# Performance work log

Measured on AMD Instinct MI355X. Metric: run time of the kernel, lower is better.

Reference implementation:

```python
import jax, jax.numpy as jnp
import numpy as np

N = 100000   # nodes
E = 1600000  # edges (avg degree 16)
D = 128      # input feature dim
H = 128      # Config.hidden_dim
G = 64       # graphs in batch
OUT = 2      # output classes


def setup_inputs() -> dict:
    key = jax.random.key(0)
    ks = jax.random.split(key, 12)
    s = 0.05
    return {
        "x": jax.random.normal(ks[0], (N, D), dtype=jnp.float32),
        "edge_index": jax.random.randint(ks[1], (2, E), 0, N),
        "batch": jnp.sort(jax.random.randint(ks[2], (N,), 0, G)),
        "W1": jax.random.normal(ks[3], (H, D), dtype=jnp.float32) * s,
        "b1": jnp.zeros((H,), jnp.float32),
        "W2": jax.random.normal(ks[4], (H, H), dtype=jnp.float32) * s,
        "b2": jnp.zeros((H,), jnp.float32),
        "Wf1": jax.random.normal(ks[5], (H, H), dtype=jnp.float32) * s,
        "bf1": jnp.zeros((H,), jnp.float32),
        "Wf2": jax.random.normal(ks[6], (OUT, H), dtype=jnp.float32) * s,
        "bf2": jnp.zeros((OUT,), jnp.float32),
    }


def _gnn_layer(x, src, dst, W, b):
    # message(x_j) = Linear(x[src]); linear commutes with gather, so transform
    # node features once (N rows) instead of per-edge (E rows): same math.
    xw = x @ W.T + b                                   # [N, H]
    msg = xw[src]                                      # [E, H] gather
    summed = jax.ops.segment_sum(msg, dst, num_segments=N)            # [N, H]
    cnt = jax.ops.segment_sum(jnp.ones((src.shape[0],), x.dtype), dst,
                              num_segments=N)                          # [N]
    return summed / jnp.maximum(cnt, 1.0)[:, None]     # scatter-mean (0 for deg-0)


def reference(x, edge_index, batch, W1, b1, W2, b2, Wf1, bf1, Wf2, bf2):
    src, dst = edge_index[0], edge_index[1]
    h = jax.nn.relu(_gnn_layer(x, src, dst, W1, b1))
    h = jax.nn.relu(_gnn_layer(h, src, dst, W2, b2))
    g = jax.ops.segment_max(h, batch, num_segments=G)  # global_max_pool [G, H]
    z = jax.nn.relu(g @ Wf1.T + bf1)                   # fc (dropout = identity, eval)
    z = z @ Wf2.T + bf2                                # [G, OUT]
    return jax.nn.log_softmax(z, axis=1)
```

## Files before the change

### kernel.cpp

```cpp
#include <hip/hip_runtime.h>
#include <hip/hip_fp16.h>
#include <math.h>


#define SPLIT 16
#define BUCKET_SHIFT 8
#define BUCKET_SIZE 256
#define MAXBUCK 512
#define BIN_CHUNK 4096
#define CAP 4608
#define LSTR 136

typedef _Float16 half8 __attribute__((ext_vector_type(8)));
typedef _Float16 half4v __attribute__((ext_vector_type(4)));
typedef _Float16 half2v __attribute__((ext_vector_type(2)));
typedef float floatx4 __attribute__((ext_vector_type(4)));
typedef float floatx2 __attribute__((ext_vector_type(2)));

#define RFL(v) __builtin_amdgcn_readfirstlane(v)

__global__ void k_init(int* bcur, int* gstart, int* gend, int G, int nbuck) {
    int i = threadIdx.x;
    if (i < nbuck) bcur[i] = i * CAP;
    if (i < G) { gstart[i] = 0; gend[i] = 0; }
}

__global__ __launch_bounds__(256) void k_bin(
        const int* __restrict__ src, const int* __restrict__ dst,
        int* __restrict__ bcur, int* __restrict__ staging,
        const int* __restrict__ batch, int* __restrict__ gstart,
        int* __restrict__ gend, int E, int N, int nbuck) {
    __shared__ int lh[MAXBUCK];
    __shared__ int lbase[MAXBUCK];
    __shared__ int lc[MAXBUCK];
    int t = threadIdx.x;
    for (int i = t; i < nbuck; i += 256) { lh[i] = 0; lc[i] = 0; }

    int n = blockIdx.x * 256 + t;
    if (n < N) {
        int b = batch[n];
        if (n == 0 || batch[n - 1] != b) gstart[b] = n;
        if (n == N - 1 || batch[n + 1] != b) gend[b] = n + 1;
    }
    __syncthreads();

    int base = blockIdx.x * BIN_CHUNK;
    if (base + BIN_CHUNK <= E) {
        int ds[16], ss[16];
        const int4* dv = (const int4*)(dst + base);
        const int4* sv = (const int4*)(src + base);
        #pragma unroll
        for (int j = 0; j < 4; ++j) {
            int4 d = dv[j * 256 + t];
            int4 s = sv[j * 256 + t];
            ds[j * 4 + 0] = d.x; ds[j * 4 + 1] = d.y;
            ds[j * 4 + 2] = d.z; ds[j * 4 + 3] = d.w;
            ss[j * 4 + 0] = s.x; ss[j * 4 + 1] = s.y;
            ss[j * 4 + 2] = s.z; ss[j * 4 + 3] = s.w;
        }
        #pragma unroll
        for (int q = 0; q < 16; ++q)
            atomicAdd(&lh[ds[q] >> BUCKET_SHIFT], 1);
        __syncthreads();
        for (int i = t; i < nbuck; i += 256)
            if (lh[i]) lbase[i] = atomicAdd(&bcur[i], lh[i]);
        __syncthreads();
        #pragma unroll
        for (int q = 0; q < 16; ++q) {
            int d = ds[q];
            int b = d >> BUCKET_SHIFT;
            int pos = lbase[b] + atomicAdd(&lc[b], 1);
            if (pos < (b + 1) * CAP)
                staging[pos] = ss[q] | ((d & (BUCKET_SIZE - 1)) << 24);
        }
    } else {
        int end = E;
        for (int e = base + t; e < end; e += 256)
            atomicAdd(&lh[dst[e] >> BUCKET_SHIFT], 1);
        __syncthreads();
        for (int i = t; i < nbuck; i += 256)
            if (lh[i]) lbase[i] = atomicAdd(&bcur[i], lh[i]);
        __syncthreads();
        for (int e = base + t; e < end; e += 256) {
            int d = dst[e];
            int b = d >> BUCKET_SHIFT;
            int pos = lbase[b] + atomicAdd(&lc[b], 1);
            if (pos < (b + 1) * CAP)
                staging[pos] = src[e] | ((d & (BUCKET_SIZE - 1)) << 24);
        }
    }
}

__global__ __launch_bounds__(BUCKET_SIZE) void k_bcsr(
        const int* __restrict__ staging, const int* __restrict__ bcur,
        int* __restrict__ esrc, int* __restrict__ rowstart,
        int* __restrict__ deg, int N) {
    __shared__ int lh[BUCKET_SIZE];
    __shared__ int lcur[BUCKET_SIZE];
    __shared__ int ws[4];
    int b = blockIdx.x;
    int s = b * CAP;
    int e = min(bcur[b], s + CAP);
    int t = threadIdx.x;
    lh[t] = 0;
    __syncthreads();
    for (int i = s + t; i < e; i += BUCKET_SIZE)
        atomicAdd(&lh[((unsigned)staging[i]) >> 24], 1);
    __syncthreads();
    int v = lh[t];
    int lane = t & 63;
    int wv = t >> 6;
    int inc = v;
    #pragma unroll
    for (int off = 1; off < 64; off <<= 1) {
        int x = __shfl_up(inc, off, 64);
        if (lane >= off) inc += x;
    }
    if (lane == 63) ws[wv] = inc;
    __syncthreads();
    int woff = 0;
    #pragma unroll
    for (int k = 0; k < 3; ++k)
        if (k < wv) woff += ws[k];
    int excl = woff + inc - v;
    int node = b * BUCKET_SIZE + t;
    if (node < N) { rowstart[node] = s + excl; deg[node] = v; }
    lcur[t] = excl;
    __syncthreads();
    for (int i = s + t; i < e; i += BUCKET_SIZE) {
        int p = staging[i];
        int local = ((unsigned)p) >> 24;
        int pos = atomicAdd(&lcur[local], 1);
        esrc[s + pos] = p & 0xFFFFFF;
    }
}

template <typename T>
__global__ __launch_bounds__(512) void k_gemm(const T* __restrict__ in,
                                              const float* __restrict__ W,
                                              const float* __restrict__ bias,
                                              unsigned char* __restrict__ out8,
                                              int N) {
    __shared__ _Float16 sX[128 * LSTR];
    __shared__ _Float16 sW[128 * LSTR];
    int t = threadIdx.x;
    int n0 = blockIdx.x * 128;

    #pragma unroll
    for (int it = 0; it < 8; ++it) {
        int lin = it * 512 + t;
        int r = lin >> 5;
        int c = (lin & 31) * 4;
        half4v xh;
        int n = n0 + r;
        if (n < N) {
            if constexpr (sizeof(T) == 4) {
                float4 xv = *(const float4*)((const float*)in + (size_t)n * 128 + c);
                xh = half4v{ (_Float16)xv.x, (_Float16)xv.y, (_Float16)xv.z, (_Float16)xv.w };
            } else {
                xh = *(const half4v*)((const _Float16*)in + (size_t)n * 128 + c);
            }
        } else {
            xh = half4v{ 0, 0, 0, 0 };
        }
        float4 wv = *(const float4*)(W + r * 128 + c);
        half4v wh = { (_Float16)wv.x, (_Float16)wv.y, (_Float16)wv.z, (_Float16)wv.w };
        *(half4v*)&sX[r * LSTR + c] = xh;
        *(half4v*)&sW[r * LSTR + c] = wh;
    }
    __syncthreads();

    int w = t >> 6;
    int lane = t & 63;
    int quad = lane >> 4;
    int lrow = lane & 15;

    floatx4 acc[8];
    #pragma unroll
    for (int i = 0; i < 8; ++i) acc[i] = {0.f, 0.f, 0.f, 0.f};

    int arow = (w * 16 + lrow) * LSTR + quad * 8;
    #pragma unroll
    for (int k0 = 0; k0 < 128; k0 += 32) {
        half8 a = *(const half8*)&sX[arow + k0];
        #pragma unroll
        for (int ht = 0; ht < 8; ++ht) {
            half8 b = *(const half8*)&sW[(ht * 16 + lrow) * LSTR + quad * 8 + k0];
            acc[ht] = __builtin_amdgcn_mfma_f32_16x16x32_f16(a, b, acc[ht], 0, 0, 0);
        }
    }

    #pragma unroll
    for (int ht = 0; ht < 8; ++ht) {
        int h = ht * 16 + lrow;
        float bv = bias[h];
        #pragma unroll
        for (int r = 0; r < 4; ++r) {
            int node = n0 + w * 16 + quad * 4 + r;
            if (node < N) {
                float v = acc[ht][r] + bv;
                int pk = __builtin_amdgcn_cvt_pk_fp8_f32(v, v, 0, false);
                out8[(size_t)node * 128 + h] = (unsigned char)(pk & 0xFF);
            }
        }
    }
}

__global__ __launch_bounds__(256) void k_agg(const unsigned char* __restrict__ in8,
                                             const int* __restrict__ esrc,
                                             const int* __restrict__ rowstart,
                                             const int* __restrict__ deg,
                                             _Float16* __restrict__ outh, int N) {
    int lane = threadIdx.x & 63;
    int node = blockIdx.x * 4 + (threadIdx.x >> 6);
    if (node >= N) return;
    int start = RFL(rowstart[node]);
    int d     = RFL(deg[node]);
    const unsigned short* in16 = (const unsigned short*)in8;

    floatx2 a0 = {0.f, 0.f}, a1 = {0.f, 0.f}, a2 = {0.f, 0.f}, a3 = {0.f, 0.f};

    int i = 0;
    for (; i + 8 <= d; i += 8) {
        int x0 = RFL(esrc[start + i + 0]);
        int x1 = RFL(esrc[start + i + 1]);
        int x2 = RFL(esrc[start + i + 2]);
        int x3 = RFL(esrc[start + i + 3]);
        int x4 = RFL(esrc[start + i + 4]);
        int x5 = RFL(esrc[start + i + 5]);
        int x6 = RFL(esrc[start + i + 6]);
        int x7 = RFL(esrc[start + i + 7]);
        unsigned u0 = in16[((size_t)x0 << 6) + lane];
        unsigned u1 = in16[((size_t)x1 << 6) + lane];
        unsigned u2 = in16[((size_t)x2 << 6) + lane];
        unsigned u3 = in16[((size_t)x3 << 6) + lane];
        unsigned u4 = in16[((size_t)x4 << 6) + lane];
        unsigned u5 = in16[((size_t)x5 << 6) + lane];
        unsigned u6 = in16[((size_t)x6 << 6) + lane];
        unsigned u7 = in16[((size_t)x7 << 6) + lane];
        floatx2 f0 = __builtin_amdgcn_cvt_pk_f32_fp8(u0, false);
        floatx2 f1 = __builtin_amdgcn_cvt_pk_f32_fp8(u1, false);
        floatx2 f2 = __builtin_amdgcn_cvt_pk_f32_fp8(u2, false);
        floatx2 f3 = __builtin_amdgcn_cvt_pk_f32_fp8(u3, false);
        floatx2 f4 = __builtin_amdgcn_cvt_pk_f32_fp8(u4, false);
        floatx2 f5 = __builtin_amdgcn_cvt_pk_f32_fp8(u5, false);
        floatx2 f6 = __builtin_amdgcn_cvt_pk_f32_fp8(u6, false);
        floatx2 f7 = __builtin_amdgcn_cvt_pk_f32_fp8(u7, false);
        a0.x += f0.x; a0.y += f0.y;  a1.x += f1.x; a1.y += f1.y;
        a2.x += f2.x; a2.y += f2.y;  a3.x += f3.x; a3.y += f3.y;
        a0.x += f4.x; a0.y += f4.y;  a1.x += f5.x; a1.y += f5.y;
        a2.x += f6.x; a2.y += f6.y;  a3.x += f7.x; a3.y += f7.y;
    }
    for (; i + 4 <= d; i += 4) {
        int x0 = RFL(esrc[start + i + 0]);
        int x1 = RFL(esrc[start + i + 1]);
        int x2 = RFL(esrc[start + i + 2]);
        int x3 = RFL(esrc[start + i + 3]);
        unsigned u0 = in16[((size_t)x0 << 6) + lane];
        unsigned u1 = in16[((size_t)x1 << 6) + lane];
        unsigned u2 = in16[((size_t)x2 << 6) + lane];
        unsigned u3 = in16[((size_t)x3 << 6) + lane];
        floatx2 f0 = __builtin_amdgcn_cvt_pk_f32_fp8(u0, false);
        floatx2 f1 = __builtin_amdgcn_cvt_pk_f32_fp8(u1, false);
        floatx2 f2 = __builtin_amdgcn_cvt_pk_f32_fp8(u2, false);
        floatx2 f3 = __builtin_amdgcn_cvt_pk_f32_fp8(u3, false);
        a0.x += f0.x; a0.y += f0.y;  a1.x += f1.x; a1.y += f1.y;
        a2.x += f2.x; a2.y += f2.y;  a3.x += f3.x; a3.y += f3.y;
    }
    for (; i < d; ++i) {
        int x0 = RFL(esrc[start + i]);
        unsigned u0 = in16[((size_t)x0 << 6) + lane];
        floatx2 f0 = __builtin_amdgcn_cvt_pk_f32_fp8(u0, false);
        a0.x += f0.x; a0.y += f0.y;
    }

    float sx = (a0.x + a1.x) + (a2.x + a3.x);
    float sy = (a0.y + a1.y) + (a2.y + a3.y);
    float dm = fmaxf((float)d, 1.0f);
    half2v r = { (_Float16)fmaxf(sx / dm, 0.f),
                 (_Float16)fmaxf(sy / dm, 0.f) };
    *(half2v*)(outh + (size_t)node * 128 + lane * 2) = r;
}

__global__ void k_pool1(const _Float16* __restrict__ h, const int* __restrict__ gstart,
                        const int* __restrict__ gend, float* __restrict__ pm, int G) {
    int g = blockIdx.x / SPLIT;
    int c = blockIdx.x % SPLIT;
    int t = threadIdx.x;
    int s = gstart[g], e = gend[g];
    int len = e - s;
    int chunk = (len + SPLIT - 1) / SPLIT;
    int lo = s + c * chunk;
    int hi = min(lo + chunk, e);
    float m = -INFINITY;
    for (int n = lo; n < hi; ++n)
        m = fmaxf(m, (float)h[(size_t)n * 128 + t]);
    pm[((size_t)g * SPLIT + c) * 128 + t] = m;
}

__global__ void k_fc(const float* __restrict__ pm,
                     const float* __restrict__ Wf1, const float* __restrict__ bf1,
                     const float* __restrict__ Wf2, const float* __restrict__ bf2,
                     float* __restrict__ out) {
    __shared__ float sg[128];
    __shared__ float sz[128];
    __shared__ float so[2];
    int g = blockIdx.x;
    int t = threadIdx.x;
    float m = -INFINITY;
    #pragma unroll
    for (int c = 0; c < SPLIT; ++c)
        m = fmaxf(m, pm[((size_t)g * SPLIT + c) * 128 + t]);
    sg[t] = m;
    __syncthreads();
    float z = bf1[t];
    #pragma unroll 4
    for (int d = 0; d < 128; ++d)
        z += sg[d] * Wf1[t * 128 + d];
    sz[t] = fmaxf(z, 0.f);
    __syncthreads();
    if (t < 2) {
        float o = bf2[t];
        for (int d = 0; d < 128; ++d)
            o += sz[d] * Wf2[t * 128 + d];
        so[t] = o;
    }
    __syncthreads();
    if (t == 0) {
        float a = so[0], b = so[1];
        float mx = fmaxf(a, b);
        float ls = mx + logf(expf(a - mx) + expf(b - mx));
        out[g * 2 + 0] = a - ls;
        out[g * 2 + 1] = b - ls;
    }
}

extern "C" void kernel_launch(void* const* d_in, const int* in_sizes, int n_in,
                              void* d_out, int out_size, void* d_ws, size_t ws_size,
                              hipStream_t stream) {
    const float* x   = (const float*)d_in[0];
    const int*   ei  = (const int*)d_in[1];
    const int* batch = (const int*)d_in[2];
    const float* W1  = (const float*)d_in[3];
    const float* b1  = (const float*)d_in[4];
    const float* W2  = (const float*)d_in[5];
    const float* b2  = (const float*)d_in[6];
    const float* Wf1 = (const float*)d_in[7];
    const float* bf1 = (const float*)d_in[8];
    const float* Wf2 = (const float*)d_in[9];
    const float* bf2 = (const float*)d_in[10];

    int N = in_sizes[2];
    int E = in_sizes[1] / 2;
    int G = out_size / 2;
    const int* src = ei;
    const int* dst = ei + E;
    int nbuck = (N + BUCKET_SIZE - 1) / BUCKET_SIZE;

    char* p = (char*)d_ws;
    auto alloc = [&](size_t bytes) -> char* {
        char* r = p;
        p += (bytes + 255) & ~(size_t)255;
        return r;
    };
    unsigned char* A = (unsigned char*)alloc((size_t)N * 128);
    _Float16* B    = (_Float16*)alloc((size_t)N * 128 * 2);
    int* deg       = (int*)alloc((size_t)N * 4);
    int* rowstart  = (int*)alloc((size_t)N * 4);
    int* esrc      = (int*)alloc((size_t)nbuck * CAP * 4);
    int* staging   = (int*)alloc((size_t)nbuck * CAP * 4);
    int* bcur      = (int*)alloc((MAXBUCK + 2) * 4);
    int* gstart    = (int*)alloc((size_t)G * 4);
    int* gend      = (int*)alloc((size_t)G * 4);
    float* pm      = (float*)alloc((size_t)G * SPLIT * 128 * 4);

    int nchunk = (E + BIN_CHUNK - 1) / BIN_CHUNK;

    k_init<<<1, MAXBUCK, 0, stream>>>(bcur, gstart, gend, G, nbuck);
    k_bin<<<nchunk, 256, 0, stream>>>(src, dst, bcur, staging, batch,
                                      gstart, gend, E, N, nbuck);
    k_bcsr<<<nbuck, BUCKET_SIZE, 0, stream>>>(staging, bcur, esrc, rowstart, deg, N);

    k_gemm<float><<<(N + 127) / 128, 512, 0, stream>>>(x, W1, b1, A, N);
    k_agg<<<(N + 3) / 4, 256, 0, stream>>>(A, esrc, rowstart, deg, B, N);
    k_gemm<_Float16><<<(N + 127) / 128, 512, 0, stream>>>(B, W2, b2, A, N);
    k_agg<<<(N + 3) / 4, 256, 0, stream>>>(A, esrc, rowstart, deg, B, N);
    k_pool1<<<G * SPLIT, 128, 0, stream>>>(B, gstart, gend, pm, G);
    k_fc<<<G, 128, 0, stream>>>(pm, Wf1, bf1, Wf2, bf2, (float*)d_out);
}
```

Baseline: 296.9 us.

## Pre-convert weights to fp16, tile two node blocks per GEMM, stage CSR bucket in LDS

k_init now also converts W1 and W2 to fp16 once, and the GEMM blocks read those half weights, loading them into shared memory once for two 128-node tiles. k_bcsr caches each bucket's staging entries in shared memory so global memory is read only once, and pooling uses a larger split with an unrolled max loop. These changes target repeated weight conversion, redundant global reads and low parallelism in pooling. In exchange there are fewer GEMM blocks, more LDS use in k_bcsr (lower occupancy), and more partial maxima for k_fc to reduce.

```diff
diff --git a/kernel.cpp b/kernel.cpp
--- a/kernel.cpp
+++ b/kernel.cpp
@@ -3,7 +3,7 @@
 #include <math.h>
 
 
-#define SPLIT 16
+#define SPLIT 64
 #define BUCKET_SHIFT 8
 #define BUCKET_SIZE 256
 #define MAXBUCK 512
@@ -19,10 +19,16 @@
 
 #define RFL(v) __builtin_amdgcn_readfirstlane(v)
 
-__global__ void k_init(int* bcur, int* gstart, int* gend, int G, int nbuck) {
-    int i = threadIdx.x;
+__global__ void k_init(int* __restrict__ bcur, int* __restrict__ gstart,
+                       int* __restrict__ gend,
+                       const float* __restrict__ W1, const float* __restrict__ W2,
+                       _Float16* __restrict__ w1h, _Float16* __restrict__ w2h,
+                       int G, int nbuck) {
+    int i = blockIdx.x * blockDim.x + threadIdx.x;
     if (i < nbuck) bcur[i] = i * CAP;
     if (i < G) { gstart[i] = 0; gend[i] = 0; }
+    w1h[i] = (_Float16)W1[i];
+    w2h[i] = (_Float16)W2[i];
 }
 
 __global__ __launch_bounds__(256) void k_bin(
@@ -74,14 +80,13 @@
                 staging[pos] = ss[q] | ((d & (BUCKET_SIZE - 1)) << 24);
         }
     } else {
-        int end = E;
-        for (int e = base + t; e < end; e += 256)
+        for (int e = base + t; e < E; e += 256)
             atomicAdd(&lh[dst[e] >> BUCKET_SHIFT], 1);
         __syncthreads();
         for (int i = t; i < nbuck; i += 256)
             if (lh[i]) lbase[i] = atomicAdd(&bcur[i], lh[i]);
         __syncthreads();
-        for (int e = base + t; e < end; e += 256) {
+        for (int e = base + t; e < E; e += 256) {
             int d = dst[e];
             int b = d >> BUCKET_SHIFT;
             int pos = lbase[b] + atomicAdd(&lc[b], 1);
@@ -95,17 +100,22 @@
         const int* __restrict__ staging, const int* __restrict__ bcur,
         int* __restrict__ esrc, int* __restrict__ rowstart,
         int* __restrict__ deg, int N) {
+    __shared__ int sw[CAP];
     __shared__ int lh[BUCKET_SIZE];
     __shared__ int lcur[BUCKET_SIZE];
-    __shared__ int ws[4];
+    __shared__ int wsum[4];
     int b = blockIdx.x;
     int s = b * CAP;
     int e = min(bcur[b], s + CAP);
+    int len = e - s;
     int t = threadIdx.x;
     lh[t] = 0;
     __syncthreads();
-    for (int i = s + t; i < e; i += BUCKET_SIZE)
-        atomicAdd(&lh[((unsigned)staging[i]) >> 24], 1);
+    for (int i = t; i < len; i += BUCKET_SIZE) {
+        int p = staging[s + i];
+        sw[i] = p;
+        atomicAdd(&lh[((unsigned)p) >> 24], 1);
+    }
     __syncthreads();
     int v = lh[t];
     int lane = t & 63;
@@ -116,19 +126,19 @@
         int x = __shfl_up(inc, off, 64);
         if (lane >= off) inc += x;
     }
-    if (lane == 63) ws[wv] = inc;
+    if (lane == 63) wsum[wv] = inc;
     __syncthreads();
     int woff = 0;
     #pragma unroll
     for (int k = 0; k < 3; ++k)
-        if (k < wv) woff += ws[k];
+        if (k < wv) woff += wsum[k];
     int excl = woff + inc - v;
     int node = b * BUCKET_SIZE + t;
     if (node < N) { rowstart[node] = s + excl; deg[node] = v; }
     lcur[t] = excl;
     __syncthreads();
-    for (int i = s + t; i < e; i += BUCKET_SIZE) {
-        int p = staging[i];
+    for (int i = t; i < len; i += BUCKET_SIZE) {
+        int p = sw[i];
         int local = ((unsigned)p) >> 24;
         int pos = atomicAdd(&lcur[local], 1);
         esrc[s + pos] = p & 0xFFFFFF;
@@ -137,70 +147,79 @@
 
 template <typename T>
 __global__ __launch_bounds__(512) void k_gemm(const T* __restrict__ in,
-                                              const float* __restrict__ W,
+                                              const _Float16* __restrict__ Wh,
                                               const float* __restrict__ bias,
                                               unsigned char* __restrict__ out8,
                                               int N) {
     __shared__ _Float16 sX[128 * LSTR];
     __shared__ _Float16 sW[128 * LSTR];
     int t = threadIdx.x;
-    int n0 = blockIdx.x * 128;
 
     #pragma unroll
     for (int it = 0; it < 8; ++it) {
         int lin = it * 512 + t;
         int r = lin >> 5;
         int c = (lin & 31) * 4;
-        half4v xh;
-        int n = n0 + r;
-        if (n < N) {
-            if constexpr (sizeof(T) == 4) {
-                float4 xv = *(const float4*)((const float*)in + (size_t)n * 128 + c);
-                xh = half4v{ (_Float16)xv.x, (_Float16)xv.y, (_Float16)xv.z, (_Float16)xv.w };
-            } else {
-                xh = *(const half4v*)((const _Float16*)in + (size_t)n * 128 + c);
-            }
-        } else {
-            xh = half4v{ 0, 0, 0, 0 };
-        }
-        float4 wv = *(const float4*)(W + r * 128 + c);
-        half4v wh = { (_Float16)wv.x, (_Float16)wv.y, (_Float16)wv.z, (_Float16)wv.w };
-        *(half4v*)&sX[r * LSTR + c] = xh;
-        *(half4v*)&sW[r * LSTR + c] = wh;
-    }
-    __syncthreads();
+        *(half4v*)&sW[r * LSTR + c] = *(const half4v*)(Wh + r * 128 + c);
+    }
 
     int w = t >> 6;
     int lane = t & 63;
     int quad = lane >> 4;
     int lrow = lane & 15;
 
-    floatx4 acc[8];
     #pragma unroll
-    for (int i = 0; i < 8; ++i) acc[i] = {0.f, 0.f, 0.f, 0.f};
-
-    int arow = (w * 16 + lrow) * LSTR + quad * 8;
-    #pragma unroll
-    for (int k0 = 0; k0 < 128; k0 += 32) {
-        half8 a = *(const half8*)&sX[arow + k0];
+    for (int tile = 0; tile < 2; ++tile) {
+        int n0 = blockIdx.x * 256 + tile * 128;
+        __syncthreads();
+        #pragma unroll
+        for (int it = 0; it < 8; ++it) {
+            int lin = it * 512 + t;
+            int r = lin >> 5;
+            int c = (lin & 31) * 4;
+            half4v xh;
+            int n = n0 + r;
+            if (n < N) {
+                if constexpr (sizeof(T) == 4) {
+                    float4 xv = *(const float4*)((const float*)in + (size_t)n * 128 + c);
+                    xh = half4v{ (_Float16)xv.x, (_Float16)xv.y, (_Float16)xv.z, (_Float16)xv.w };
+                } else {
+                    xh = *(const half4v*)((const _Float16*)in + (size_t)n * 128 + c);
+                }
+            } else {
+                xh = half4v{ 0, 0, 0, 0 };
+            }
+            *(half4v*)&sX[r * LSTR + c] = xh;
+        }
+        __syncthreads();
+
+        floatx4 acc[8];
+        #pragma unroll
+        for (int i = 0; i < 8; ++i) acc[i] = {0.f, 0.f, 0.f, 0.f};
+
+        int arow = (w * 16 + lrow) * LSTR + quad * 8;
+        #pragma unroll
+        for (int k0 = 0; k0 < 128; k0 += 32) {
+            half8 a = *(const half8*)&sX[arow + k0];
+            #pragma unroll
+            for (int ht = 0; ht < 8; ++ht) {
+                half8 bfr = *(const half8*)&sW[(ht * 16 + lrow) * LSTR + quad * 8 + k0];
+                acc[ht] = __builtin_amdgcn_mfma_f32_16x16x32_f16(a, bfr, acc[ht], 0, 0, 0);
+            }
+        }
+
         #pragma unroll
         for (int ht = 0; ht < 8; ++ht) {
-            half8 b = *(const half8*)&sW[(ht * 16 + lrow) * LSTR + quad * 8 + k0];
-            acc[ht] = __builtin_amdgcn_mfma_f32_16x16x32_f16(a, b, acc[ht], 0, 0, 0);
-        }
-    }
-
-    #pragma unroll
-    for (int ht = 0; ht < 8; ++ht) {
-        int h = ht * 16 + lrow;
-        float bv = bias[h];
-        #pragma unroll
-        for (int r = 0; r < 4; ++r) {
-            int node = n0 + w * 16 + quad * 4 + r;
-            if (node < N) {
-                float v = acc[ht][r] + bv;
-                int pk = __builtin_amdgcn_cvt_pk_fp8_f32(v, v, 0, false);
-                out8[(size_t)node * 128 + h] = (unsigned char)(pk & 0xFF);
+            int h = ht * 16 + lrow;
+            float bv = bias[h];
+            #pragma unroll
+            for (int r = 0; r < 4; ++r) {
+                int node = n0 + w * 16 + quad * 4 + r;
+                if (node < N) {
+                    float v = acc[ht][r] + bv;
+                    int pk = __builtin_amdgcn_cvt_pk_fp8_f32(v, v, 0, false);
+                    out8[(size_t)node * 128 + h] = (unsigned char)(pk & 0xFF);
+                }
             }
         }
     }
@@ -293,7 +312,21 @@
     int lo = s + c * chunk;
     int hi = min(lo + chunk, e);
     float m = -INFINITY;
-    for (int n = lo; n < hi; ++n)
+    int n = lo;
+    for (; n + 8 <= hi; n += 8) {
+        float v0 = (float)h[(size_t)(n + 0) * 128 + t];
+        float v1 = (float)h[(size_t)(n + 1) * 128 + t];
+        float v2 = (float)h[(size_t)(n + 2) * 128 + t];
+        float v3 = (float)h[(size_t)(n + 3) * 128 + t];
+        float v4 = (float)h[(size_t)(n + 4) * 128 + t];
+        float v5 = (float)h[(size_t)(n + 5) * 128 + t];
+        float v6 = (float)h[(size_t)(n + 6) * 128 + t];
+        float v7 = (float)h[(size_t)(n + 7) * 128 + t];
+        float m0 = fmaxf(fmaxf(v0, v1), fmaxf(v2, v3));
+        float m1 = fmaxf(fmaxf(v4, v5), fmaxf(v6, v7));
+        m = fmaxf(m, fmaxf(m0, m1));
+    }
+    for (; n < hi; ++n)
         m = fmaxf(m, (float)h[(size_t)n * 128 + t]);
     pm[((size_t)g * SPLIT + c) * 128 + t] = m;
 }
@@ -308,7 +341,7 @@
     int g = blockIdx.x;
     int t = threadIdx.x;
     float m = -INFINITY;
-    #pragma unroll
+    #pragma unroll 8
     for (int c = 0; c < SPLIT; ++c)
         m = fmaxf(m, pm[((size_t)g * SPLIT + c) * 128 + t]);
     sg[t] = m;
@@ -373,17 +406,19 @@
     int* gstart    = (int*)alloc((size_t)G * 4);
     int* gend      = (int*)alloc((size_t)G * 4);
     float* pm      = (float*)alloc((size_t)G * SPLIT * 128 * 4);
+    _Float16* w1h  = (_Float16*)alloc((size_t)128 * 128 * 2);
+    _Float16* w2h  = (_Float16*)alloc((size_t)128 * 128 * 2);
 
     int nchunk = (E + BIN_CHUNK - 1) / BIN_CHUNK;
 
-    k_init<<<1, MAXBUCK, 0, stream>>>(bcur, gstart, gend, G, nbuck);
+    k_init<<<64, 256, 0, stream>>>(bcur, gstart, gend, W1, W2, w1h, w2h, G, nbuck);
     k_bin<<<nchunk, 256, 0, stream>>>(src, dst, bcur, staging, batch,
                                       gstart, gend, E, N, nbuck);
     k_bcsr<<<nbuck, BUCKET_SIZE, 0, stream>>>(staging, bcur, esrc, rowstart, deg, N);
 
-    k_gemm<float><<<(N + 127) / 128, 512, 0, stream>>>(x, W1, b1, A, N);
+    k_gemm<float><<<(N + 255) / 256, 512, 0, stream>>>(x, w1h, b1, A, N);
     k_agg<<<(N + 3) / 4, 256, 0, stream>>>(A, esrc, rowstart, deg, B, N);
-    k_gemm<_Float16><<<(N + 127) / 128, 512, 0, stream>>>(B, W2, b2, A, N);
+    k_gemm<_Float16><<<(N + 255) / 256, 512, 0, stream>>>(B, w2h, b2, A, N);
     k_agg<<<(N + 3) / 4, 256, 0, stream>>>(A, esrc, rowstart, deg, B, N);
     k_pool1<<<G * SPLIT, 128, 0, stream>>>(B, gstart, gend, pm, G);
     k_fc<<<G, 128, 0, stream>>>(pm, Wf1, bf1, Wf2, bf2, (float*)d_out);
```

After: 291.0 us. 2.0% less time.
